# Performance work log

Measured on AMD Instinct MI355X. Metric: run time of the kernel, lower is better.

The kernel has to match this reference:

```python
import jax, jax.numpy as jnp
import numpy as np

B, S, N_STATE, N_HEAD = 8, 4096, 1024, 16
N_FREQ = 10000.0
H_DIM = N_STATE // N_HEAD          # 64
N_ROTS = H_DIM // 2                # 32


def setup_inputs() -> dict:
    key = jax.random.key(0)
    k1, k2, k3, k4, k5 = jax.random.split(key, 5)
    x = jax.random.normal(k1, (B, S, N_STATE), dtype=jnp.float32)
    # rotation angles (module inits to zeros; small random values exercise the math)
    thetas = jax.random.normal(k2, (N_ROTS,), dtype=jnp.float32) * 0.1
    # r_pairs.long() in torch -> integer plane indices; ensure i != j
    i = jax.random.randint(k3, (N_ROTS,), 0, H_DIM)
    off = jax.random.randint(k4, (N_ROTS,), 1, H_DIM)
    j = (i + off) % H_DIM
    r_pairs = jnp.stack([i, j], axis=-1).astype(jnp.int32)
    theta_scale = jnp.ones((1,), dtype=jnp.float32)
    # r_matrix inits to identity; add small noise so it is non-trivial
    r_matrix = jnp.eye(H_DIM, dtype=jnp.float32) + 0.01 * jax.random.normal(k5, (H_DIM, H_DIM), dtype=jnp.float32)
    inv_freq = 1.0 / (N_FREQ ** (jnp.arange(0, H_DIM, 2, dtype=jnp.float32) / H_DIM))
    return {"x": x, "thetas": thetas, "theta_scale": theta_scale,
            "r_matrix": r_matrix, "inv_freq": inv_freq,
            "r_pairs": r_pairs, "n_head": N_HEAD}


def reference(x, thetas, theta_scale, r_matrix, inv_freq, r_pairs, n_head):
    b, s, n_state = x.shape
    h_dim = n_state // n_head
    x2d = x.reshape(-1, h_dim)  # [B*S*H, h_dim]
    angles = thetas * theta_scale[0]

    # Sequential Givens plane rotations: x @ G(i,j,theta) only touches columns i, j.
    def step(carry, inp):
        theta, ij = inp
        i, j = ij[0], ij[1]
        c, sn = jnp.cos(theta), jnp.sin(theta)
        xi = carry[:, i]
        xj = carry[:, j]
        carry = carry.at[:, i].set(xi * c + xj * sn)
        carry = carry.at[:, j].set(-xi * sn + xj * c)
        return carry, None

    x2d, _ = jax.lax.scan(step, x2d, (angles, r_pairs))
    x2d = x2d @ r_matrix
    xh = x2d.reshape(b, s, n_head, h_dim)

    # RoPE-style sin/cos mix
    pos = jnp.arange(s, dtype=jnp.float32)
    sinu = pos[:, None] * inv_freq[None, :]          # [s, h_dim//2]
    sin = jnp.sin(sinu)[None, :, None, :]
    cos = jnp.cos(sinu)[None, :, None, :]
    x1, x2 = xh[..., ::2], xh[..., 1::2]
    out = jnp.concatenate([x1 * cos - x2 * sin, x1 * sin + x2 * cos], axis=-1)
    return out.reshape(b, s, n_state)
```

## Files before the change

### kernel.cpp

```cpp
#include <hip/hip_runtime.h>
#include <cstdint>
#include <cstddef>

#define S_LEN   4096
#define NROT    32
#define NGRP    8192

typedef __attribute__((ext_vector_type(8))) short  short8x;
typedef __attribute__((ext_vector_type(4))) float  floatx4;

typedef __attribute__((address_space(1))) unsigned int gu32;
typedef __attribute__((address_space(3))) unsigned int lu32;

__device__ __host__ inline unsigned short f2bf(float f) {
  union { float f; unsigned u; } c; c.f = f;
  unsigned u = c.u;
  return (unsigned short)((u + 0x7fffu + ((u >> 16) & 1u)) >> 16);
}
__device__ inline float bf2f(unsigned short h) {
  union { unsigned u; float f; } c; c.u = ((unsigned)h) << 16;
  return c.f;
}

__global__ void setup_kernel(const float* __restrict__ thetas,
                             const float* __restrict__ theta_scale,
                             const float* __restrict__ r_matrix,
                             const int*   __restrict__ r_pairs,
                             const float* __restrict__ inv_freq,
                             uint4* __restrict__ Bfrag,
                             float2* __restrict__ csT) {
  if (blockIdx.x < 512) {
    int idx = blockIdx.x * 256 + threadIdx.x;
    int s = idx >> 5;
    int f = idx & 31;
    float ang = (float)s * inv_freq[f];
    csT[idx] = make_float2(cosf(ang), sinf(ang));
    return;
  }
  __shared__ float C[64 * 65];
  __shared__ float Mm[64 * 64];
  int tid = threadIdx.x;
  if (tid < 64) {
    for (int c = 0; c < 64; ++c) C[tid * 65 + c] = (tid == c) ? 1.0f : 0.0f;
    float sc = theta_scale[0];
    for (int q = 0; q < NROT; ++q) {
      float th = thetas[q] * sc;
      float cs = cosf(th), sn = sinf(th);
      int i = r_pairs[2 * q], j = r_pairs[2 * q + 1];
      float xi = C[tid * 65 + i];
      float xj = C[tid * 65 + j];
      C[tid * 65 + i] =  xi * cs + xj * sn;
      C[tid * 65 + j] = -xi * sn + xj * cs;
    }
  }
  __syncthreads();
  for (int o = tid; o < 64 * 64; o += 256) {
    int t = o >> 6, c = o & 63;
    float a = 0.0f;
    for (int k = 0; k < 64; ++k) a = fmaf(C[t * 65 + k], r_matrix[k * 64 + c], a);
    Mm[o] = a;
  }
  __syncthreads();
  for (int e = tid; e < 8 * 64; e += 256) {
    int f = e >> 6, l = e & 63;
    int ks = f & 1, nt = f >> 1;
    int col = nt * 16 + (l & 15);
    unsigned short w[8];
    for (int j = 0; j < 8; ++j) {
      int k = ks * 32 + (l >> 4) * 8 + j;
      w[j] = f2bf(Mm[k * 64 + col]);
    }
    uint4 pk;
    pk.x = (unsigned)w[0] | ((unsigned)w[1] << 16);
    pk.y = (unsigned)w[2] | ((unsigned)w[3] << 16);
    pk.z = (unsigned)w[4] | ((unsigned)w[5] << 16);
    pk.w = (unsigned)w[6] | ((unsigned)w[7] << 16);
    Bfrag[e] = pk;
  }
}

__global__ __launch_bounds__(256)
void rotary_main(const float* __restrict__ x,
                 const uint4* __restrict__ Bfrag,
                 const float2* __restrict__ csT,
                 float* __restrict__ out) {
  __shared__ float sstage[4][2][1024];
  __shared__ uint4 sB[8 * 64];
  const int tid  = threadIdx.x;
  const int lane = tid & 63;
  const int wid  = tid >> 6;
  const int g    = blockIdx.x * 4 + wid;

  const int lr = lane & 15;
  const int lk = lane >> 4;

  #pragma unroll
  for (int i = 0; i < 2; ++i) {
    const int chunk = wid * 2 + i;
    __builtin_amdgcn_global_load_lds(
        (gu32*)(const void*)(Bfrag + chunk * 64 + lane),
        (lu32*)(void*)(sB + chunk * 64), 16, 0, 0);
  }
  const int s0 = (g * 4) & (S_LEN - 1);
  float4 cs[4], rt[4];
  #pragma unroll
  for (int nt = 0; nt < 4; ++nt) {
    cs[nt] = *(const float4*)(csT + s0 * 32 + nt * 8 + lk * 2);
    rt[nt] = *(const float4*)(csT + 32 + nt * 8 + lk * 2);
  }
  __syncthreads();

  const float* xg = x + (size_t)g * 4096;
  float* og = out + (size_t)g * 4096;
  float* stg = &sstage[wid][0][0];

  #define STAGE(t, b) {                                                     \
    float* dst_ = stg + (b) * 1024;                                         \
    _Pragma("unroll")                                                       \
    for (int q_ = 0; q_ < 4; ++q_) {                                        \
      const int row_ = q_ * 4 + lk;                                         \
      const int gs_  = lr ^ (row_ & 7);                                     \
      __builtin_amdgcn_global_load_lds(                                     \
        (gu32*)(const void*)(xg + (size_t)((t) * 16 + row_) * 64 + gs_ * 4),\
        (lu32*)(void*)(dst_ + q_ * 256), 16, 0, 0);                         \
    }                                                                       \
  }

  STAGE(0, 0)
  STAGE(1, 1)
  __builtin_amdgcn_sched_barrier(0);

  const short8x* sBf = (const short8x*)sB;
  const int key  = lr & 7;
  const int okey = key << 2;

  #pragma unroll
  for (int t = 0; t < 4; ++t) {
    if (t == 0)      { asm volatile("s_waitcnt vmcnt(4)"  ::: "memory"); }
    else if (t == 1) { asm volatile("s_waitcnt vmcnt(8)"  ::: "memory"); }
    else if (t == 2) { asm volatile("s_waitcnt vmcnt(12)" ::: "memory"); }
    else             { asm volatile("s_waitcnt vmcnt(8)"  ::: "memory"); }
    __builtin_amdgcn_sched_barrier(0);

    float* buf = stg + (t & 1) * 1024;

    const float* bb = buf + lr * 64;
    floatx4 x0 = *(const floatx4*)(bb + (((lk * 2 + 0)    ) ^ key) * 4);
    floatx4 x1 = *(const floatx4*)(bb + (((lk * 2 + 1)    ) ^ key) * 4);
    floatx4 x2 = *(const floatx4*)(bb + (((lk * 2 + 0) + 8) ^ key) * 4);
    floatx4 x3 = *(const floatx4*)(bb + (((lk * 2 + 1) + 8) ^ key) * 4);

    short8x Xh0, Xl0, Xh1, Xl1;
    #pragma unroll
    for (int i = 0; i < 8; ++i) {
      float v0 = (i < 4) ? x0[i] : x1[i - 4];
      float v1 = (i < 4) ? x2[i] : x3[i - 4];
      unsigned u0 = __builtin_bit_cast(unsigned, v0);
      unsigned u1 = __builtin_bit_cast(unsigned, v1);
      unsigned short h0 = (unsigned short)(u0 >> 16);
      unsigned short h1 = (unsigned short)(u1 >> 16);
      Xh0[i] = (short)h0; Xl0[i] = (short)f2bf(v0 - bf2f(h0));
      Xh1[i] = (short)h1; Xl1[i] = (short)f2bf(v1 - bf2f(h1));
    }

    #pragma unroll
    for (int nt = 0; nt < 4; ++nt) {
      short8x bh0 = sBf[(nt * 2 + 0) * 64 + lane];
      short8x bh1 = sBf[(nt * 2 + 1) * 64 + lane];

      floatx4 acc0 = {0.f, 0.f, 0.f, 0.f};
      floatx4 acc1 = {0.f, 0.f, 0.f, 0.f};
      acc0 = __builtin_amdgcn_mfma_f32_16x16x32_bf16(bh0, Xh0, acc0, 0, 0, 0);
      acc1 = __builtin_amdgcn_mfma_f32_16x16x32_bf16(bh1, Xh1, acc1, 0, 0, 0);
      acc0 = __builtin_amdgcn_mfma_f32_16x16x32_bf16(bh0, Xl0, acc0, 0, 0, 0);
      acc1 = __builtin_amdgcn_mfma_f32_16x16x32_bf16(bh1, Xl1, acc1, 0, 0, 0);

      const float a0  = acc0[0] + acc1[0];
      const float b0v = acc0[1] + acc1[1];
      const float a1  = acc0[2] + acc1[2];
      const float b1v = acc0[3] + acc1[3];
      float2 ev, od;
      ev.x = fmaf(a0, cs[nt].x, -(b0v * cs[nt].y));
      ev.y = fmaf(a1, cs[nt].z, -(b1v * cs[nt].w));
      od.x = fmaf(a0, cs[nt].y,   b0v * cs[nt].x);
      od.y = fmaf(a1, cs[nt].w,   b1v * cs[nt].z);
      float* ow = buf + lr * 64;
      *(float2*)(ow + ((     nt * 8 + lk * 2) ^ okey)) = ev;
      *(float2*)(ow + ((32 + nt * 8 + lk * 2) ^ okey)) = od;
    }

    if (t < 3) {
      #pragma unroll
      for (int nt = 0; nt < 4; ++nt) {
        float c0 = cs[nt].x, s0v = cs[nt].y, c1 = cs[nt].z, s1v = cs[nt].w;
        cs[nt].x = fmaf(c0, rt[nt].x, -(s0v * rt[nt].y));
        cs[nt].y = fmaf(c0, rt[nt].y,   s0v * rt[nt].x);
        cs[nt].z = fmaf(c1, rt[nt].z, -(s1v * rt[nt].w));
        cs[nt].w = fmaf(c1, rt[nt].w,   s1v * rt[nt].z);
      }
    }

    asm volatile("s_waitcnt lgkmcnt(0)" ::: "memory");
    __builtin_amdgcn_sched_barrier(0);
    floatx4 vr[4];
    #pragma unroll
    for (int q = 0; q < 4; ++q) {
      const int row = q * 4 + lk;
      vr[q] = *(const floatx4*)(buf + row * 64 + ((lr * 4) ^ ((row & 7) << 2)));
    }
    asm volatile("s_waitcnt lgkmcnt(0)" ::: "memory");
    __builtin_amdgcn_sched_barrier(0);
    if (t < 2) STAGE(t + 2, t & 1)
    __builtin_amdgcn_sched_barrier(0);
    #pragma unroll
    for (int q = 0; q < 4; ++q) {
      const int row = q * 4 + lk;
      *(floatx4*)(og + (size_t)(t * 16 + row) * 64 + lr * 4) = vr[q];
    }
  }
  #undef STAGE
}

extern "C" void kernel_launch(void* const* d_in, const int* in_sizes, int n_in,
                              void* d_out, int out_size, void* d_ws, size_t ws_size,
                              hipStream_t stream) {
  const float* x           = (const float*)d_in[0];
  const float* thetas      = (const float*)d_in[1];
  const float* theta_scale = (const float*)d_in[2];
  const float* r_matrix    = (const float*)d_in[3];
  const float* inv_freq    = (const float*)d_in[4];
  const int*   r_pairs     = (const int*)d_in[5];

  uint4*  Bfrag = (uint4*)d_ws;
  float2* csT   = (float2*)((char*)d_ws + 16384);
  float*  outp  = (float*)d_out;

  setup_kernel<<<513, 256, 0, stream>>>(thetas, theta_scale, r_matrix, r_pairs,
                                        inv_freq, Bfrag, csT);
  rotary_main<<<NGRP / 4, 256, 0, stream>>>(x, Bfrag, csT, outp);
}
```

Baseline: 73.65 us.

## Single-buffer LDS staging and load cos/sin table per step instead of recurrence

Replaces the per-wave double-buffered LDS staging with a single 4 KB buffer, so each wave prefetches only the next tile after draining the current one and waits with vmcnt(0). This halves LDS use per block, which should let more blocks fit per CU and gain occupancy. The cos/sin factors are now read from the precomputed table for every position, replacing the angle-addition recurrence and its extra registers. The cost is less overlap inside a wave: the full vmcnt(0) wait also covers outstanding stores, and each step adds four more global loads.

```diff
diff --git a/kernel.cpp b/kernel.cpp
--- a/kernel.cpp
+++ b/kernel.cpp
@@ -84,7 +84,7 @@
                  const uint4* __restrict__ Bfrag,
                  const float2* __restrict__ csT,
                  float* __restrict__ out) {
-  __shared__ float sstage[4][2][1024];
+  __shared__ float sstage[4][1024];
   __shared__ uint4 sB[8 * 64];
   const int tid  = threadIdx.x;
   const int lane = tid & 63;
@@ -101,33 +101,33 @@
         (gu32*)(const void*)(Bfrag + chunk * 64 + lane),
         (lu32*)(void*)(sB + chunk * 64), 16, 0, 0);
   }
-  const int s0 = (g * 4) & (S_LEN - 1);
-  float4 cs[4], rt[4];
-  #pragma unroll
-  for (int nt = 0; nt < 4; ++nt) {
-    cs[nt] = *(const float4*)(csT + s0 * 32 + nt * 8 + lk * 2);
-    rt[nt] = *(const float4*)(csT + 32 + nt * 8 + lk * 2);
-  }
   __syncthreads();
 
   const float* xg = x + (size_t)g * 4096;
   float* og = out + (size_t)g * 4096;
-  float* stg = &sstage[wid][0][0];
-
-  #define STAGE(t, b) {                                                     \
-    float* dst_ = stg + (b) * 1024;                                         \
+  float* buf = &sstage[wid][0];
+
+  #define STAGE(t) {                                                        \
     _Pragma("unroll")                                                       \
     for (int q_ = 0; q_ < 4; ++q_) {                                        \
       const int row_ = q_ * 4 + lk;                                         \
       const int gs_  = lr ^ (row_ & 7);                                     \
       __builtin_amdgcn_global_load_lds(                                     \
         (gu32*)(const void*)(xg + (size_t)((t) * 16 + row_) * 64 + gs_ * 4),\
-        (lu32*)(void*)(dst_ + q_ * 256), 16, 0, 0);                         \
+        (lu32*)(void*)(buf + q_ * 256), 16, 0, 0);                          \
     }                                                                       \
   }
 
-  STAGE(0, 0)
-  STAGE(1, 1)
+  float4 csv[4];
+  #define LOAD_CS(t) {                                                      \
+    const int spos_ = (g * 4 + (t)) & (S_LEN - 1);                          \
+    _Pragma("unroll")                                                       \
+    for (int nt_ = 0; nt_ < 4; ++nt_)                                       \
+      csv[nt_] = *(const float4*)(csT + spos_ * 32 + nt_ * 8 + lk * 2);     \
+  }
+
+  STAGE(0)
+  LOAD_CS(0)
   __builtin_amdgcn_sched_barrier(0);
 
   const short8x* sBf = (const short8x*)sB;
@@ -136,13 +136,8 @@
 
   #pragma unroll
   for (int t = 0; t < 4; ++t) {
-    if (t == 0)      { asm volatile("s_waitcnt vmcnt(4)"  ::: "memory"); }
-    else if (t == 1) { asm volatile("s_waitcnt vmcnt(8)"  ::: "memory"); }
-    else if (t == 2) { asm volatile("s_waitcnt vmcnt(12)" ::: "memory"); }
-    else             { asm volatile("s_waitcnt vmcnt(8)"  ::: "memory"); }
-    __builtin_amdgcn_sched_barrier(0);
-
-    float* buf = stg + (t & 1) * 1024;
+    asm volatile("s_waitcnt vmcnt(0)" ::: "memory");
+    __builtin_amdgcn_sched_barrier(0);
 
     const float* bb = buf + lr * 64;
     floatx4 x0 = *(const floatx4*)(bb + (((lk * 2 + 0)    ) ^ key) * 4);
@@ -180,45 +175,33 @@
       const float a1  = acc0[2] + acc1[2];
       const float b1v = acc0[3] + acc1[3];
       float2 ev, od;
-      ev.x = fmaf(a0, cs[nt].x, -(b0v * cs[nt].y));
-      ev.y = fmaf(a1, cs[nt].z, -(b1v * cs[nt].w));
-      od.x = fmaf(a0, cs[nt].y,   b0v * cs[nt].x);
-      od.y = fmaf(a1, cs[nt].w,   b1v * cs[nt].z);
+      ev.x = fmaf(a0, csv[nt].x, -(b0v * csv[nt].y));
+      ev.y = fmaf(a1, csv[nt].z, -(b1v * csv[nt].w));
+      od.x = fmaf(a0, csv[nt].y,   b0v * csv[nt].x);
+      od.y = fmaf(a1, csv[nt].w,   b1v * csv[nt].z);
       float* ow = buf + lr * 64;
       *(float2*)(ow + ((     nt * 8 + lk * 2) ^ okey)) = ev;
       *(float2*)(ow + ((32 + nt * 8 + lk * 2) ^ okey)) = od;
     }
 
-    if (t < 3) {
-      #pragma unroll
-      for (int nt = 0; nt < 4; ++nt) {
-        float c0 = cs[nt].x, s0v = cs[nt].y, c1 = cs[nt].z, s1v = cs[nt].w;
-        cs[nt].x = fmaf(c0, rt[nt].x, -(s0v * rt[nt].y));
-        cs[nt].y = fmaf(c0, rt[nt].y,   s0v * rt[nt].x);
-        cs[nt].z = fmaf(c1, rt[nt].z, -(s1v * rt[nt].w));
-        cs[nt].w = fmaf(c1, rt[nt].w,   s1v * rt[nt].z);
-      }
-    }
-
     asm volatile("s_waitcnt lgkmcnt(0)" ::: "memory");
     __builtin_amdgcn_sched_barrier(0);
-    floatx4 vr[4];
-    #pragma unroll
-    for (int q = 0; q < 4; ++q) {
-      const int row = q * 4 + lk;
-      vr[q] = *(const floatx4*)(buf + row * 64 + ((lr * 4) ^ ((row & 7) << 2)));
-    }
+    floatx4 vr0, vr1, vr2, vr3;
+    vr0 = *(const floatx4*)(buf + (0 * 4 + lk) * 64 + ((lr * 4) ^ (((0 * 4 + lk) & 7) << 2)));
+    vr1 = *(const floatx4*)(buf + (1 * 4 + lk) * 64 + ((lr * 4) ^ (((1 * 4 + lk) & 7) << 2)));
+    vr2 = *(const floatx4*)(buf + (2 * 4 + lk) * 64 + ((lr * 4) ^ (((2 * 4 + lk) & 7) << 2)));
+    vr3 = *(const floatx4*)(buf + (3 * 4 + lk) * 64 + ((lr * 4) ^ (((3 * 4 + lk) & 7) << 2)));
     asm volatile("s_waitcnt lgkmcnt(0)" ::: "memory");
     __builtin_amdgcn_sched_barrier(0);
-    if (t < 2) STAGE(t + 2, t & 1)
-    __builtin_amdgcn_sched_barrier(0);
-    #pragma unroll
-    for (int q = 0; q < 4; ++q) {
-      const int row = q * 4 + lk;
-      *(floatx4*)(og + (size_t)(t * 16 + row) * 64 + lr * 4) = vr[q];
-    }
+    if (t < 3) { STAGE(t + 1) LOAD_CS(t + 1) }
+    __builtin_amdgcn_sched_barrier(0);
+    *(floatx4*)(og + (size_t)(t * 16 + 0 * 4 + lk) * 64 + lr * 4) = vr0;
+    *(floatx4*)(og + (size_t)(t * 16 + 1 * 4 + lk) * 64 + lr * 4) = vr1;
+    *(floatx4*)(og + (size_t)(t * 16 + 2 * 4 + lk) * 64 + lr * 4) = vr2;
+    *(floatx4*)(og + (size_t)(t * 16 + 3 * 4 + lk) * 64 + lr * 4) = vr3;
   }
   #undef STAGE
+  #undef LOAD_CS
 }
 
 extern "C" void kernel_launch(void* const* d_in, const int* in_sizes, int n_in,
```

Measured after the change: 73.88 us. No clear change (+0.3%).

## Load whole per-wave x tile into LDS upfront instead of double-buffered staging

Applied to the files above, without the earlier changes.

Replaces the two-slot double-buffered staging of x tiles with a single upfront load of all four 16-row tiles per wave into a larger LDS buffer (64 KB per block), followed by one full vmcnt(0) wait. This removes the per-iteration staged waits and the re-issue of loads inside the loop, so each tile can be processed and written back directly. In exchange, all loads must complete before any compute starts, and the larger LDS footprint may lower occupancy.

```diff
diff --git a/kernel.cpp b/kernel.cpp
--- a/kernel.cpp
+++ b/kernel.cpp
@@ -84,7 +84,7 @@
                  const uint4* __restrict__ Bfrag,
                  const float2* __restrict__ csT,
                  float* __restrict__ out) {
-  __shared__ float sstage[4][2][1024];
+  __shared__ float sstage[4][4096];
   __shared__ uint4 sB[8 * 64];
   const int tid  = threadIdx.x;
   const int lane = tid & 63;
@@ -112,22 +112,18 @@
 
   const float* xg = x + (size_t)g * 4096;
   float* og = out + (size_t)g * 4096;
-  float* stg = &sstage[wid][0][0];
-
-  #define STAGE(t, b) {                                                     \
-    float* dst_ = stg + (b) * 1024;                                         \
-    _Pragma("unroll")                                                       \
-    for (int q_ = 0; q_ < 4; ++q_) {                                        \
-      const int row_ = q_ * 4 + lk;                                         \
-      const int gs_  = lr ^ (row_ & 7);                                     \
-      __builtin_amdgcn_global_load_lds(                                     \
-        (gu32*)(const void*)(xg + (size_t)((t) * 16 + row_) * 64 + gs_ * 4),\
-        (lu32*)(void*)(dst_ + q_ * 256), 16, 0, 0);                         \
-    }                                                                       \
-  }
-
-  STAGE(0, 0)
-  STAGE(1, 1)
+  float* buf = &sstage[wid][0];
+
+  #pragma unroll
+  for (int q = 0; q < 16; ++q) {
+    const int row = q * 4 + lk;
+    const int gs  = lr ^ (row & 7);
+    __builtin_amdgcn_global_load_lds(
+        (gu32*)(const void*)(xg + (size_t)row * 64 + gs * 4),
+        (lu32*)(void*)(buf + q * 256), 16, 0, 0);
+  }
+  __builtin_amdgcn_sched_barrier(0);
+  asm volatile("s_waitcnt vmcnt(0)" ::: "memory");
   __builtin_amdgcn_sched_barrier(0);
 
   const short8x* sBf = (const short8x*)sB;
@@ -136,15 +132,9 @@
 
   #pragma unroll
   for (int t = 0; t < 4; ++t) {
-    if (t == 0)      { asm volatile("s_waitcnt vmcnt(4)"  ::: "memory"); }
-    else if (t == 1) { asm volatile("s_waitcnt vmcnt(8)"  ::: "memory"); }
-    else if (t == 2) { asm volatile("s_waitcnt vmcnt(12)" ::: "memory"); }
-    else             { asm volatile("s_waitcnt vmcnt(8)"  ::: "memory"); }
-    __builtin_amdgcn_sched_barrier(0);
-
-    float* buf = stg + (t & 1) * 1024;
-
-    const float* bb = buf + lr * 64;
+    float* qbuf = buf + t * 1024;
+
+    const float* bb = qbuf + lr * 64;
     floatx4 x0 = *(const floatx4*)(bb + (((lk * 2 + 0)    ) ^ key) * 4);
     floatx4 x1 = *(const floatx4*)(bb + (((lk * 2 + 1)    ) ^ key) * 4);
     floatx4 x2 = *(const floatx4*)(bb + (((lk * 2 + 0) + 8) ^ key) * 4);
@@ -184,7 +174,7 @@
       ev.y = fmaf(a1, cs[nt].z, -(b1v * cs[nt].w));
       od.x = fmaf(a0, cs[nt].y,   b0v * cs[nt].x);
       od.y = fmaf(a1, cs[nt].w,   b1v * cs[nt].z);
-      float* ow = buf + lr * 64;
+      float* ow = qbuf + lr * 64;
       *(float2*)(ow + ((     nt * 8 + lk * 2) ^ okey)) = ev;
       *(float2*)(ow + ((32 + nt * 8 + lk * 2) ^ okey)) = od;
     }
@@ -202,23 +192,14 @@
 
     asm volatile("s_waitcnt lgkmcnt(0)" ::: "memory");
     __builtin_amdgcn_sched_barrier(0);
-    floatx4 vr[4];
     #pragma unroll
     for (int q = 0; q < 4; ++q) {
       const int row = q * 4 + lk;
-      vr[q] = *(const floatx4*)(buf + row * 64 + ((lr * 4) ^ ((row & 7) << 2)));
-    }
-    asm volatile("s_waitcnt lgkmcnt(0)" ::: "memory");
-    __builtin_amdgcn_sched_barrier(0);
-    if (t < 2) STAGE(t + 2, t & 1)
-    __builtin_amdgcn_sched_barrier(0);
-    #pragma unroll
-    for (int q = 0; q < 4; ++q) {
-      const int row = q * 4 + lk;
-      *(floatx4*)(og + (size_t)(t * 16 + row) * 64 + lr * 4) = vr[q];
-    }
-  }
-  #undef STAGE
+      floatx4 vr = *(const floatx4*)(qbuf + row * 64 +
+                                     ((lr * 4) ^ ((row & 7) << 2)));
+      *(floatx4*)(og + (size_t)(t * 16 + row) * 64 + lr * 4) = vr;
+    }
+  }
 }
 
 extern "C" void kernel_launch(void* const* d_in, const int* in_sizes, int n_in,
```

Measured after the change: 73.46 us. No clear change (-0.3%).
